# Optimization experiments

Measured on AMD Instinct MI355X. Metric: run time of the kernel, lower is better.

Reference implementation:

```python
import math
import jax, jax.numpy as jnp
import numpy as np
from jax import lax

N, C, H, W = 16, 128, 56, 56


def _conv(x, w, padding, dilation=(1, 1), groups=1):
    # NCHW conv matching torch.nn.Conv2d semantics (bias=False)
    return lax.conv_general_dilated(
        x, w, window_strides=(1, 1),
        padding=[(padding[0], padding[0]), (padding[1], padding[1])],
        rhs_dilation=dilation,
        dimension_numbers=('NCHW', 'OIHW', 'NCHW'),
        feature_group_count=groups)


def setup_inputs() -> dict:
    key = jax.random.key(0)
    ks = jax.random.split(key, 6)
    x = jax.random.normal(ks[0], (N, C, H, W), jnp.float32)
    w2 = jax.random.normal(ks[1], (C, C, 1, 3), jnp.float32) * 0.05   # dense 1x3 conv
    p6w = jax.random.normal(ks[2], (1, C, 7, 1), jnp.float32) * 0.02  # trunc_normal std=0.02
    w7 = jax.random.normal(ks[3], (C, 1, 1, 5), jnp.float32) * 0.05   # depthwise 1x5
    w8 = jax.random.normal(ks[4], (C, 1, 5, 5), jnp.float32) * 0.05   # depthwise 5x5 dil=2
    p9w = jax.random.normal(ks[5], (1, 1, 7, C), jnp.float32) * 0.02
    return {"x": x, "w2": w2, "p6w": p6w, "w7": w7, "w8": w8, "p9w": p9w}


def reference(x, w2, p6w, w7, w8, p9w):
    n, c, h, w = x.shape
    # t_1: F.unfold(x, (1,7), dilation=(1,2), padding=(0,6)) -> (n, c, 7, h, w)
    # tap k reads column j + 2k - 6 of x (zero padded)
    xp = jnp.pad(x, ((0, 0), (0, 0), (0, 0), (6, 6)))
    t1 = jnp.stack([xp[..., 2 * k:2 * k + w] for k in range(7)], axis=2)
    # t_2: dense (1,3) conv, padding (0,1)
    t2 = _conv(x, w2, (0, 1))
    # t_3: windowed channel correlation, (n, c, 7, c)
    t3 = jnp.einsum('nakhw,nbhw->nakb', t1, x) / math.sqrt(h * w)
    # t_4: F.unfold(t_2, (7,1), padding=(3,0)) -> (n, c, 7, h, w), taps along height
    t2p = jnp.pad(t2, ((0, 0), (0, 0), (3, 3), (0, 0)))
    t4 = jnp.stack([t2p[:, :, k:k + h, :] for k in range(7)], axis=2)
    # elementwise weighting
    t6 = p6w * t3          # (1,c,7,1) broadcast over (n,c,7,c)
    # depthwise convs
    t7 = _conv(t2, w7, (0, 2), groups=c)                 # (1,5) depthwise
    t8 = _conv(x, w8, (4, 4), dilation=(2, 2), groups=c)  # (5,5) depthwise, dil 2
    t9 = p9w * t6          # (1,1,7,c) broadcast
    # t_10: contract (c_in, tap) against windowed t4 -> (n, c, h, w)
    t10 = jnp.einsum('nakb,nakhw->nbhw', t9, t4) / math.sqrt(c * 7)
    t11 = t10 - t7
    t12 = t8 - t11
    return t12
```

## Files before the change

kernel.cpp:

```cpp
#include <hip/hip_runtime.h>

#define N_ 16
#define C_ 128
#define H_ 56
#define W_ 56
#define HW_ 3136

typedef __bf16 bf16x8 __attribute__((ext_vector_type(8)));
typedef __bf16 bf16x2 __attribute__((ext_vector_type(2)));
typedef float f32x4 __attribute__((ext_vector_type(4)));

#define XT_PER_N 401408
#define T2_PLANE 3472
#define T2_PER_N 444416
#define S_PER_N 114688
#define T10_PER_N 401408

#define WS_T10_OFF   3670016u
#define WS_T3_OFF    12845056u
#define WS_T2PB_OFF  20185088u
#define WS_W2B_OFF   34406400u

__global__ __launch_bounds__(256) void w2b_prep(const float* __restrict__ w2,
                                                __bf16* __restrict__ w2b) {
    int idx = blockIdx.x * 256 + threadIdx.x;
    int co = idx / 384, kk = idx - co * 384;
    int j = kk >> 7, ci = kk & 127;
    w2b[idx] = (__bf16)w2[co * 384 + ci * 3 + j];
}

__global__ __launch_bounds__(256) void p1_transpose(const float* __restrict__ x,
                                                    __bf16* __restrict__ xT) {
    int c = blockIdx.x, n = blockIdx.y;
    __shared__ float xs[56 * 57];
    int tid = threadIdx.x;
    const float* xp = x + (size_t)(n * C_ + c) * HW_;
    for (int i = tid; i < HW_; i += 256) {
        int h = i / 56, w = i - 56 * h;
        xs[w * 57 + h] = xp[i];
    }
    __syncthreads();
    __bf16* op = xT + (size_t)(n * C_ + c) * HW_;
    for (int i = tid; i < 1568; i += 256) {
        int j = 2 * i;
        int wp = j / 56, h = j - 56 * wp;
        bf16x2 pr = {(__bf16)xs[wp * 57 + h], (__bf16)xs[wp * 57 + h + 1]};
        *(bf16x2*)&op[j] = pr;
    }
}

__global__ __launch_bounds__(256) void k1_mfma(const float* __restrict__ x,
                                               const __bf16* __restrict__ w2b,
                                               __bf16* __restrict__ t2pb) {
    int h = blockIdx.x, n = blockIdx.y;
    __shared__ __align__(16) __bf16 Bs[66 * 136];
    __shared__ __align__(16) __bf16 As[128 * 72];
    int tid = threadIdx.x;
    int wv = tid >> 6, lane = tid & 63;
    int lm = lane & 15, lq = lane >> 4;
    int wi = wv >> 1, wj = wv & 1;

    const float* xn = x + (size_t)n * C_ * HW_ + h * 56;
    for (int i = tid; i < 66 * 128; i += 256) {
        int ci = i / 66, wp = i - 66 * ci;
        int wx = wp - 1;
        float v = (wx >= 0 && wx < 56) ? xn[ci * HW_ + wx] : 0.f;
        Bs[wp * 136 + ci] = (__bf16)v;
    }

    f32x4 acc[4][2];
    f32x4 zero4 = {0.f, 0.f, 0.f, 0.f};
#pragma unroll
    for (int i = 0; i < 4; i++)
#pragma unroll
        for (int j = 0; j < 2; j++) acc[i][j] = zero4;

    const __bf16* w2n = w2b;
    for (int c6 = 0; c6 < 6; c6++) {
#pragma unroll
        for (int u = 0; u < 4; u++) {
            int v = tid + u * 256;
            int m = v & 7, co = v >> 3;
            *(bf16x8*)&As[co * 72 + 8 * m] =
                *(const bf16x8*)(w2n + co * 384 + c6 * 64 + 8 * m);
        }
        __syncthreads();
#pragma unroll
        for (int kl = 0; kl < 2; kl++) {
            int ks = c6 * 2 + kl;
            int j = ks >> 2;
            int cbase = (ks & 3) * 32;
            bf16x8 av[4], bv[2];
#pragma unroll
            for (int i = 0; i < 4; i++)
                av[i] = *(const bf16x8*)&As[(wi * 64 + i * 16 + lm) * 72 + kl * 32 + lq * 8];
#pragma unroll
            for (int jt = 0; jt < 2; jt++) {
                int row = wj * 32 + jt * 16 + lm + j;
                bv[jt] = *(const bf16x8*)&Bs[row * 136 + cbase + lq * 8];
            }
#pragma unroll
            for (int i = 0; i < 4; i++)
#pragma unroll
                for (int jt = 0; jt < 2; jt++)
                    acc[i][jt] = __builtin_amdgcn_mfma_f32_16x16x32_bf16(av[i], bv[jt], acc[i][jt], 0, 0, 0);
        }
        __syncthreads();
    }

    float* buf = (float*)As;
    __bf16* t2n = t2pb + (size_t)n * T2_PER_N;
#pragma unroll 1
    for (int i = 0; i < 4; i++) {
        __syncthreads();
#pragma unroll
        for (int jt = 0; jt < 2; jt++)
#pragma unroll
            for (int r = 0; r < 4; r++)
                buf[(wi * 16 + lq * 4 + r) * 65 + wj * 32 + jt * 16 + lm] = acc[i][jt][r];
        __syncthreads();
        int row = tid >> 3, seg = tid & 7;
        if (seg < 7) {
            int co = (row < 16) ? (i * 16 + row) : (64 + i * 16 + (row - 16));
            const float* src = &buf[row * 65 + seg * 8];
            bf16x8 o8;
#pragma unroll
            for (int d = 0; d < 8; d++) o8[d] = (__bf16)src[d];
            *(bf16x8*)(t2n + (size_t)co * T2_PLANE + (h + 3) * 56 + seg * 8) = o8;
        }
    }
}

__global__ __launch_bounds__(256) void k2_mfma(const __bf16* __restrict__ xT,
                                               float* __restrict__ t3) {
    int hc = blockIdx.x, k = blockIdx.y, n = blockIdx.z;
    __shared__ __align__(16) __bf16 As[128 * 72];
    __shared__ __align__(16) __bf16 Bs[128 * 72];
    int tid = threadIdx.x;
    int wv = tid >> 6, lane = tid & 63;
    int lm = lane & 15, lq = lane >> 4;
    int wi = wv >> 1, wj = wv & 1;

    f32x4 acc[4][4];
    f32x4 zero4 = {0.f, 0.f, 0.f, 0.f};
#pragma unroll
    for (int i = 0; i < 4; i++)
#pragma unroll
        for (int j = 0; j < 4; j++) acc[i][j] = zero4;

    const __bf16* xTn = xT + (size_t)n * XT_PER_N;
    __bf16 bz = (__bf16)0.f;
    bf16x8 vzero = {bz, bz, bz, bz, bz, bz, bz, bz};

    for (int ci = 0; ci < 14; ci++) {
        int w = hc * 14 + ci;
        int wpA = w + 2 * k - 6;
        bool aval = (wpA >= 0 && wpA < 56);
#pragma unroll
        for (int u = 0; u < 4; u++) {
            int v = tid + u * 256;
            int m = v & 7, a = v >> 3;
            bf16x8 va = vzero, vb = vzero;
            if (m < 7) {
                if (aval) va = *(const bf16x8*)(xTn + (a * 56 + wpA) * 56 + 8 * m);
                vb = *(const bf16x8*)(xTn + (a * 56 + w) * 56 + 8 * m);
            }
            *(bf16x8*)&As[a * 72 + 8 * m] = va;
            *(bf16x8*)&Bs[a * 72 + 8 * m] = vb;
        }
        __syncthreads();
#pragma unroll
        for (int kb = 0; kb < 2; kb++) {
            bf16x8 av[4], bv[4];
#pragma unroll
            for (int i = 0; i < 4; i++)
                av[i] = *(const bf16x8*)&As[(wi * 64 + i * 16 + lm) * 72 + kb * 32 + lq * 8];
#pragma unroll
            for (int j = 0; j < 4; j++)
                bv[j] = *(const bf16x8*)&Bs[(wj * 64 + j * 16 + lm) * 72 + kb * 32 + lq * 8];
#pragma unroll
            for (int i = 0; i < 4; i++)
#pragma unroll
                for (int j = 0; j < 4; j++)
                    acc[i][j] = __builtin_amdgcn_mfma_f32_16x16x32_bf16(av[i], bv[j], acc[i][j], 0, 0, 0);
        }
        __syncthreads();
    }

    float* t3p = t3 + (size_t)(n * 7 + k) * (C_ * C_);
    const float inv56 = 1.0f / 56.0f;
#pragma unroll
    for (int i = 0; i < 4; i++)
#pragma unroll
        for (int j = 0; j < 4; j++)
#pragma unroll
            for (int r = 0; r < 4; r++) {
                int a = wi * 64 + i * 16 + lq * 4 + r;
                int b = wj * 64 + j * 16 + lm;
                atomicAdd(&t3p[a * C_ + b], acc[i][j][r] * inv56);
            }
}

__global__ __launch_bounds__(256) void sprep(const float* __restrict__ t3,
                                             const float* __restrict__ p6w,
                                             const float* __restrict__ p9w,
                                             __bf16* __restrict__ s) {
    int idx = blockIdx.x * 256 + threadIdx.x;
    int n = idx / S_PER_N;
    int rem = idx - n * S_PER_N;
    int b = rem / 896;
    int ak = rem - b * 896;
    int a = ak / 7, k = ak - 7 * a;
    const float rs = 0.03340766f;
    float v = t3[((size_t)(n * 7 + k) * C_ + a) * C_ + b] * p6w[a * 7 + k] *
              p9w[k * C_ + b] * rs;
    s[idx] = (__bf16)v;
}

__global__ __launch_bounds__(256) void k3_mfma(const __bf16* __restrict__ s,
                                               const __bf16* __restrict__ t2pb,
                                               __bf16* __restrict__ t10) {
    int tile = blockIdx.x;
    int n = blockIdx.y;
    int hw0 = tile * 64;
    __shared__ __align__(16) __bf16 As[128 * 72];
    __shared__ __align__(16) __bf16 Bs[64 * 72];
    int tid = threadIdx.x;
    int wv = tid >> 6, lane = tid & 63;
    int lm = lane & 15, lq = lane >> 4;
    int wi = wv >> 1, wj = wv & 1;

    f32x4 acc[4][2];
    f32x4 zero4 = {0.f, 0.f, 0.f, 0.f};
#pragma unroll
    for (int i = 0; i < 4; i++)
#pragma unroll
        for (int j = 0; j < 2; j++) acc[i][j] = zero4;

    const __bf16* s_n = s + (size_t)n * S_PER_N;
    const __bf16* t2n = t2pb + (size_t)n * T2_PER_N;

    for (int kb = 0; kb < 14; kb++) {
#pragma unroll
        for (int u = 0; u < 4; u++) {
            int v = tid + u * 256;
            int m = v & 7, b = v >> 3;
            *(bf16x8*)&As[b * 72 + 8 * m] =
                *(const bf16x8*)(s_n + b * 896 + kb * 64 + 8 * m);
        }
        {
            int o = tid & 7;
            int p = tid >> 3;
            int ak0 = kb * 64 + 2 * p;
            int a0 = ak0 / 7, k0 = ak0 - 7 * a0;
            int ak1 = ak0 + 1;
            int a1 = ak1 / 7, k1 = ak1 - 7 * a1;
            int hwg = hw0 + 8 * o;
            bf16x8 v0 = *(const bf16x8*)(t2n + a0 * T2_PLANE + hwg + 56 * k0);
            bf16x8 v1 = *(const bf16x8*)(t2n + a1 * T2_PLANE + hwg + 56 * k1);
            int g = p >> 2;
            int off = (2 * p) & 7;
            int phys = ((g ^ o) << 3) + off;
#pragma unroll
            for (int j = 0; j < 8; j++) {
                int row = 8 * o + j;
                bf16x2 pr = {v0[j], v1[j]};
                *(bf16x2*)&Bs[row * 72 + phys] = pr;
            }
        }
        __syncthreads();
#pragma unroll
        for (int kbi = 0; kbi < 2; kbi++) {
            bf16x8 av[4], bv[2];
#pragma unroll
            for (int i = 0; i < 4; i++)
                av[i] = *(const bf16x8*)&As[(wi * 64 + i * 16 + lm) * 72 + kbi * 32 + lq * 8];
#pragma unroll
            for (int j = 0; j < 2; j++) {
                int row = wj * 32 + j * 16 + lm;
                int g = kbi * 4 + lq;
                int pg = g ^ (row >> 3);
                bv[j] = *(const bf16x8*)&Bs[row * 72 + pg * 8];
            }
#pragma unroll
            for (int i = 0; i < 4; i++)
#pragma unroll
                for (int j = 0; j < 2; j++)
                    acc[i][j] = __builtin_amdgcn_mfma_f32_16x16x32_bf16(av[i], bv[j], acc[i][j], 0, 0, 0);
        }
        __syncthreads();
    }

    float* buf = (float*)As;
    __bf16* t10n = t10 + (size_t)n * T10_PER_N;
#pragma unroll 1
    for (int i = 0; i < 4; i++) {
        __syncthreads();
#pragma unroll
        for (int j = 0; j < 2; j++)
#pragma unroll
            for (int r = 0; r < 4; r++)
                buf[(wi * 16 + lq * 4 + r) * 65 + wj * 32 + j * 16 + lm] = acc[i][j][r];
        __syncthreads();
        int row = tid >> 3, seg = tid & 7;
        int b = (row < 16) ? (i * 16 + row) : (64 + i * 16 + (row - 16));
        const float* src = &buf[row * 65 + seg * 8];
        bf16x8 o8;
#pragma unroll
        for (int d = 0; d < 8; d++) o8[d] = (__bf16)src[d];
        *(bf16x8*)(t10n + (size_t)b * HW_ + hw0 + seg * 8) = o8;
    }
}

__global__ __launch_bounds__(256) void d_final(const float* __restrict__ x,
                                               const __bf16* __restrict__ t2pb,
                                               const __bf16* __restrict__ t10,
                                               const float* __restrict__ w7,
                                               const float* __restrict__ w8,
                                               float* __restrict__ out) {
    int b = blockIdx.x, n = blockIdx.y;
    __shared__ float xs[64 * 65];
    __shared__ float t2s[56 * 60];
    int tid = threadIdx.x;
    const float* xp = x + (size_t)(n * C_ + b) * HW_;
    for (int i = tid; i < 64 * 65; i += 256) {
        int hh = i / 65, ww = i - 65 * hh;
        int h = hh - 4, w = ww - 4;
        float v = (h >= 0 && h < 56 && w >= 0 && w < 56) ? xp[h * 56 + w] : 0.f;
        xs[i] = v;
    }
    const __bf16* t2p = t2pb + (size_t)(n * C_ + b) * T2_PLANE;
    for (int i = tid; i < 56 * 60; i += 256) {
        int h = i / 60, ww = i - 60 * h;
        int w = ww - 2;
        float v = (w >= 0 && w < 56) ? (float)t2p[(h + 3) * 56 + w] : 0.f;
        t2s[i] = v;
    }
    __syncthreads();

    int r = tid >> 2;
    if (r >= 56) return;
    int w0 = (tid & 3) * 14;

    float w7r[5], w8r[25];
#pragma unroll
    for (int q = 0; q < 5; q++) w7r[q] = w7[b * 5 + q];
#pragma unroll
    for (int q = 0; q < 25; q++) w8r[q] = w8[b * 25 + q];

    float acc[14];
    {
        float tw[18];
#pragma unroll
        for (int c = 0; c < 18; c++) tw[c] = t2s[r * 60 + w0 + c];
#pragma unroll
        for (int i = 0; i < 14; i++)
            acc[i] = tw[i] * w7r[0] + tw[i + 1] * w7r[1] + tw[i + 2] * w7r[2] +
                     tw[i + 3] * w7r[3] + tw[i + 4] * w7r[4];
    }
#pragma unroll
    for (int p = 0; p < 5; p++) {
        float xv[22];
        int base = (r + 2 * p) * 65 + w0;
#pragma unroll
        for (int c = 0; c < 22; c++) xv[c] = xs[base + c];
#pragma unroll
        for (int i = 0; i < 14; i++)
            acc[i] += xv[i] * w8r[p * 5 + 0] + xv[i + 2] * w8r[p * 5 + 1] +
                      xv[i + 4] * w8r[p * 5 + 2] + xv[i + 6] * w8r[p * 5 + 3] +
                      xv[i + 8] * w8r[p * 5 + 4];
    }
    const __bf16* t10r = t10 + (size_t)(n * C_ + b) * HW_ + r * 56 + w0;
    float* outr = out + (size_t)(n * C_ + b) * HW_ + r * 56 + w0;
#pragma unroll
    for (int i = 0; i < 14; i++) outr[i] = acc[i] - (float)t10r[i];
}

extern "C" void kernel_launch(void* const* d_in, const int* in_sizes, int n_in,
                              void* d_out, int out_size, void* d_ws, size_t ws_size,
                              hipStream_t stream) {
    const float* x = (const float*)d_in[0];
    const float* w2 = (const float*)d_in[1];
    const float* p6w = (const float*)d_in[2];
    const float* w7 = (const float*)d_in[3];
    const float* w8 = (const float*)d_in[4];
    const float* p9w = (const float*)d_in[5];
    float* outp = (float*)d_out;

    char* ws = (char*)d_ws;
    __bf16* xT = (__bf16*)ws;
    __bf16* s = (__bf16*)ws;
    __bf16* t10 = (__bf16*)(ws + WS_T10_OFF);
    float* t3 = (float*)(ws + WS_T3_OFF);
    __bf16* t2pb = (__bf16*)(ws + WS_T2PB_OFF);
    __bf16* w2b = (__bf16*)(ws + WS_W2B_OFF);

    hipMemsetAsync(t2pb, 0, (size_t)N_ * C_ * T2_PLANE * sizeof(__bf16), stream);
    hipMemsetAsync(t3, 0, (size_t)N_ * 7 * C_ * C_ * sizeof(float), stream);

    w2b_prep<<<dim3(192), 256, 0, stream>>>(w2, w2b);
    p1_transpose<<<dim3(C_, N_), 256, 0, stream>>>(x, xT);
    k1_mfma<<<dim3(H_, N_), 256, 0, stream>>>(x, w2b, t2pb);
    k2_mfma<<<dim3(4, 7, N_), 256, 0, stream>>>(xT, t3);
    sprep<<<dim3((N_ * S_PER_N) / 256), 256, 0, stream>>>(t3, p6w, p9w, s);
    k3_mfma<<<dim3(49, N_), 256, 0, stream>>>(s, t2pb, t10);
    d_final<<<dim3(C_, N_), 256, 0, stream>>>(x, t2pb, t10, w7, w8, outp);
}
```

Baseline: 233.0 us.

## Load MFMA operands directly from global memory and double-buffer k3 B tiles

k1 and k3 now read the A operand (weights or s) straight from global memory into registers instead of staging it through LDS, which removes several barriers. k2 drops LDS staging entirely and walks only the valid, non-padded columns as a flat contiguous range per shift k, doubling the grid to 8 chunks per (k,n). k3 also double-buffers the transposed t2 B tile so the next tile loads while the current one computes. The cost is more uncached-pattern global loads per wave, plus more atomic adds into t3 from the larger k2 grid.

```diff
diff --git a/kernel.cpp b/kernel.cpp
--- a/kernel.cpp
+++ b/kernel.cpp
@@ -54,7 +54,7 @@
                                                __bf16* __restrict__ t2pb) {
     int h = blockIdx.x, n = blockIdx.y;
     __shared__ __align__(16) __bf16 Bs[66 * 136];
-    __shared__ __align__(16) __bf16 As[128 * 72];
+    __shared__ __align__(16) float kbuf[32 * 65];
     int tid = threadIdx.x;
     int wv = tid >> 6, lane = tid & 63;
     int lm = lane & 15, lq = lane >> 4;
@@ -67,6 +67,7 @@
         float v = (wx >= 0 && wx < 56) ? xn[ci * HW_ + wx] : 0.f;
         Bs[wp * 136 + ci] = (__bf16)v;
     }
+    __syncthreads();
 
     f32x4 acc[4][2];
     f32x4 zero4 = {0.f, 0.f, 0.f, 0.f};
@@ -75,40 +76,26 @@
 #pragma unroll
         for (int j = 0; j < 2; j++) acc[i][j] = zero4;
 
-    const __bf16* w2n = w2b;
-    for (int c6 = 0; c6 < 6; c6++) {
-#pragma unroll
-        for (int u = 0; u < 4; u++) {
-            int v = tid + u * 256;
-            int m = v & 7, co = v >> 3;
-            *(bf16x8*)&As[co * 72 + 8 * m] =
-                *(const bf16x8*)(w2n + co * 384 + c6 * 64 + 8 * m);
-        }
-        __syncthreads();
-#pragma unroll
-        for (int kl = 0; kl < 2; kl++) {
-            int ks = c6 * 2 + kl;
-            int j = ks >> 2;
-            int cbase = (ks & 3) * 32;
-            bf16x8 av[4], bv[2];
-#pragma unroll
-            for (int i = 0; i < 4; i++)
-                av[i] = *(const bf16x8*)&As[(wi * 64 + i * 16 + lm) * 72 + kl * 32 + lq * 8];
-#pragma unroll
-            for (int jt = 0; jt < 2; jt++) {
-                int row = wj * 32 + jt * 16 + lm + j;
-                bv[jt] = *(const bf16x8*)&Bs[row * 136 + cbase + lq * 8];
-            }
-#pragma unroll
-            for (int i = 0; i < 4; i++)
-#pragma unroll
-                for (int jt = 0; jt < 2; jt++)
-                    acc[i][jt] = __builtin_amdgcn_mfma_f32_16x16x32_bf16(av[i], bv[jt], acc[i][jt], 0, 0, 0);
-        }
-        __syncthreads();
-    }
-
-    float* buf = (float*)As;
+#pragma unroll 4
+    for (int ks = 0; ks < 12; ks++) {
+        int j = ks >> 2;
+        int cbase = (ks & 3) * 32;
+        bf16x8 av[4], bv[2];
+#pragma unroll
+        for (int i = 0; i < 4; i++)
+            av[i] = *(const bf16x8*)(w2b + (wi * 64 + i * 16 + lm) * 384 + ks * 32 + lq * 8);
+#pragma unroll
+        for (int jt = 0; jt < 2; jt++) {
+            int row = wj * 32 + jt * 16 + lm + j;
+            bv[jt] = *(const bf16x8*)&Bs[row * 136 + cbase + lq * 8];
+        }
+#pragma unroll
+        for (int i = 0; i < 4; i++)
+#pragma unroll
+            for (int jt = 0; jt < 2; jt++)
+                acc[i][jt] = __builtin_amdgcn_mfma_f32_16x16x32_bf16(av[i], bv[jt], acc[i][jt], 0, 0, 0);
+    }
+
     __bf16* t2n = t2pb + (size_t)n * T2_PER_N;
 #pragma unroll 1
     for (int i = 0; i < 4; i++) {
@@ -117,12 +104,12 @@
         for (int jt = 0; jt < 2; jt++)
 #pragma unroll
             for (int r = 0; r < 4; r++)
-                buf[(wi * 16 + lq * 4 + r) * 65 + wj * 32 + jt * 16 + lm] = acc[i][jt][r];
+                kbuf[(wi * 16 + lq * 4 + r) * 65 + wj * 32 + jt * 16 + lm] = acc[i][jt][r];
         __syncthreads();
         int row = tid >> 3, seg = tid & 7;
         if (seg < 7) {
             int co = (row < 16) ? (i * 16 + row) : (64 + i * 16 + (row - 16));
-            const float* src = &buf[row * 65 + seg * 8];
+            const float* src = &kbuf[row * 65 + seg * 8];
             bf16x8 o8;
 #pragma unroll
             for (int d = 0; d < 8; d++) o8[d] = (__bf16)src[d];
@@ -134,8 +121,13 @@
 __global__ __launch_bounds__(256) void k2_mfma(const __bf16* __restrict__ xT,
                                                float* __restrict__ t3) {
     int hc = blockIdx.x, k = blockIdx.y, n = blockIdx.z;
-    __shared__ __align__(16) __bf16 As[128 * 72];
-    __shared__ __align__(16) __bf16 Bs[128 * 72];
+    int w_lo = 6 - 2 * k; if (w_lo < 0) w_lo = 0;
+    int w_hi = 62 - 2 * k; if (w_hi > 56) w_hi = 56;
+    int jlo = w_lo * 56;
+    int L = (w_hi - w_lo) * 56;
+    int T = (L + 63) >> 6;
+    int shiftA = (2 * k - 6) * 56;
+
     int tid = threadIdx.x;
     int wv = tid >> 6, lane = tid & 63;
     int lm = lane & 15, lq = lane >> 4;
@@ -152,39 +144,34 @@
     __bf16 bz = (__bf16)0.f;
     bf16x8 vzero = {bz, bz, bz, bz, bz, bz, bz, bz};
 
-    for (int ci = 0; ci < 14; ci++) {
-        int w = hc * 14 + ci;
-        int wpA = w + 2 * k - 6;
-        bool aval = (wpA >= 0 && wpA < 56);
-#pragma unroll
-        for (int u = 0; u < 4; u++) {
-            int v = tid + u * 256;
-            int m = v & 7, a = v >> 3;
-            bf16x8 va = vzero, vb = vzero;
-            if (m < 7) {
-                if (aval) va = *(const bf16x8*)(xTn + (a * 56 + wpA) * 56 + 8 * m);
-                vb = *(const bf16x8*)(xTn + (a * 56 + w) * 56 + 8 * m);
-            }
-            *(bf16x8*)&As[a * 72 + 8 * m] = va;
-            *(bf16x8*)&Bs[a * 72 + 8 * m] = vb;
-        }
-        __syncthreads();
+    const __bf16* Arow[4];
+    const __bf16* Brow[4];
+#pragma unroll
+    for (int i = 0; i < 4; i++)
+        Arow[i] = xTn + (size_t)(wi * 64 + i * 16 + lm) * HW_ + jlo + shiftA + lq * 8;
+#pragma unroll
+    for (int j = 0; j < 4; j++)
+        Brow[j] = xTn + (size_t)(wj * 64 + j * 16 + lm) * HW_ + jlo + lq * 8;
+
+    for (int c = hc; c < T; c += 8) {
+        int base = c * 64;
 #pragma unroll
         for (int kb = 0; kb < 2; kb++) {
+            int off = base + kb * 32;
+            bool val = (off + lq * 8 + 8 <= L);
             bf16x8 av[4], bv[4];
 #pragma unroll
             for (int i = 0; i < 4; i++)
-                av[i] = *(const bf16x8*)&As[(wi * 64 + i * 16 + lm) * 72 + kb * 32 + lq * 8];
+                av[i] = val ? *(const bf16x8*)(Arow[i] + off) : vzero;
 #pragma unroll
             for (int j = 0; j < 4; j++)
-                bv[j] = *(const bf16x8*)&Bs[(wj * 64 + j * 16 + lm) * 72 + kb * 32 + lq * 8];
+                bv[j] = val ? *(const bf16x8*)(Brow[j] + off) : vzero;
 #pragma unroll
             for (int i = 0; i < 4; i++)
 #pragma unroll
                 for (int j = 0; j < 4; j++)
                     acc[i][j] = __builtin_amdgcn_mfma_f32_16x16x32_bf16(av[i], bv[j], acc[i][j], 0, 0, 0);
         }
-        __syncthreads();
     }
 
     float* t3p = t3 + (size_t)(n * 7 + k) * (C_ * C_);
@@ -223,8 +210,8 @@
     int tile = blockIdx.x;
     int n = blockIdx.y;
     int hw0 = tile * 64;
-    __shared__ __align__(16) __bf16 As[128 * 72];
-    __shared__ __align__(16) __bf16 Bs[64 * 72];
+    __shared__ __align__(16) __bf16 Bs[2][64 * 72];
+    __shared__ __align__(16) float kbuf[32 * 65];
     int tid = threadIdx.x;
     int wv = tid >> 6, lane = tid & 63;
     int lm = lane & 15, lq = lane >> 4;
@@ -240,18 +227,31 @@
     const __bf16* s_n = s + (size_t)n * S_PER_N;
     const __bf16* t2n = t2pb + (size_t)n * T2_PER_N;
 
+    int o = tid & 7;
+    int p = tid >> 3;
+    {
+        int ak0 = 2 * p;
+        int a0 = ak0 / 7, k0 = ak0 - 7 * a0;
+        int ak1 = ak0 + 1;
+        int a1 = ak1 / 7, k1 = ak1 - 7 * a1;
+        int hwg = hw0 + 8 * o;
+        bf16x8 v0 = *(const bf16x8*)(t2n + a0 * T2_PLANE + hwg + 56 * k0);
+        bf16x8 v1 = *(const bf16x8*)(t2n + a1 * T2_PLANE + hwg + 56 * k1);
+        int g = p >> 2;
+        int off = (2 * p) & 7;
+        int phys = ((g ^ o) << 3) + off;
+#pragma unroll
+        for (int j = 0; j < 8; j++) {
+            int row = 8 * o + j;
+            bf16x2 pr = {v0[j], v1[j]};
+            *(bf16x2*)&Bs[0][row * 72 + phys] = pr;
+        }
+    }
+
     for (int kb = 0; kb < 14; kb++) {
-#pragma unroll
-        for (int u = 0; u < 4; u++) {
-            int v = tid + u * 256;
-            int m = v & 7, b = v >> 3;
-            *(bf16x8*)&As[b * 72 + 8 * m] =
-                *(const bf16x8*)(s_n + b * 896 + kb * 64 + 8 * m);
-        }
-        {
-            int o = tid & 7;
-            int p = tid >> 3;
-            int ak0 = kb * 64 + 2 * p;
+        __syncthreads();
+        if (kb + 1 < 14) {
+            int ak0 = (kb + 1) * 64 + 2 * p;
             int a0 = ak0 / 7, k0 = ak0 - 7 * a0;
             int ak1 = ak0 + 1;
             int a1 = ak1 / 7, k1 = ak1 - 7 * a1;
@@ -265,22 +265,22 @@
             for (int j = 0; j < 8; j++) {
                 int row = 8 * o + j;
                 bf16x2 pr = {v0[j], v1[j]};
-                *(bf16x2*)&Bs[row * 72 + phys] = pr;
+                *(bf16x2*)&Bs[(kb + 1) & 1][row * 72 + phys] = pr;
             }
         }
-        __syncthreads();
+        const __bf16* Bcur = Bs[kb & 1];
 #pragma unroll
         for (int kbi = 0; kbi < 2; kbi++) {
             bf16x8 av[4], bv[2];
 #pragma unroll
             for (int i = 0; i < 4; i++)
-                av[i] = *(const bf16x8*)&As[(wi * 64 + i * 16 + lm) * 72 + kbi * 32 + lq * 8];
+                av[i] = *(const bf16x8*)(s_n + (wi * 64 + i * 16 + lm) * 896 + kb * 64 + kbi * 32 + lq * 8);
 #pragma unroll
             for (int j = 0; j < 2; j++) {
                 int row = wj * 32 + j * 16 + lm;
                 int g = kbi * 4 + lq;
                 int pg = g ^ (row >> 3);
-                bv[j] = *(const bf16x8*)&Bs[row * 72 + pg * 8];
+                bv[j] = *(const bf16x8*)&Bcur[row * 72 + pg * 8];
             }
 #pragma unroll
             for (int i = 0; i < 4; i++)
@@ -288,10 +288,8 @@
                 for (int j = 0; j < 2; j++)
                     acc[i][j] = __builtin_amdgcn_mfma_f32_16x16x32_bf16(av[i], bv[j], acc[i][j], 0, 0, 0);
         }
-        __syncthreads();
-    }
-
-    float* buf = (float*)As;
+    }
+
     __bf16* t10n = t10 + (size_t)n * T10_PER_N;
 #pragma unroll 1
     for (int i = 0; i < 4; i++) {
@@ -300,11 +298,11 @@
         for (int j = 0; j < 2; j++)
 #pragma unroll
             for (int r = 0; r < 4; r++)
-                buf[(wi * 16 + lq * 4 + r) * 65 + wj * 32 + j * 16 + lm] = acc[i][j][r];
+                kbuf[(wi * 16 + lq * 4 + r) * 65 + wj * 32 + j * 16 + lm] = acc[i][j][r];
         __syncthreads();
         int row = tid >> 3, seg = tid & 7;
         int b = (row < 16) ? (i * 16 + row) : (64 + i * 16 + (row - 16));
-        const float* src = &buf[row * 65 + seg * 8];
+        const float* src = &kbuf[row * 65 + seg * 8];
         bf16x8 o8;
 #pragma unroll
         for (int d = 0; d < 8; d++) o8[d] = (__bf16)src[d];
@@ -401,7 +399,7 @@
     w2b_prep<<<dim3(192), 256, 0, stream>>>(w2, w2b);
     p1_transpose<<<dim3(C_, N_), 256, 0, stream>>>(x, xT);
     k1_mfma<<<dim3(H_, N_), 256, 0, stream>>>(x, w2b, t2pb);
-    k2_mfma<<<dim3(4, 7, N_), 256, 0, stream>>>(xT, t3);
+    k2_mfma<<<dim3(8, 7, N_), 256, 0, stream>>>(xT, t3);
     sprep<<<dim3((N_ * S_PER_N) / 256), 256, 0, stream>>>(t3, p6w, p9w, s);
     k3_mfma<<<dim3(49, N_), 256, 0, stream>>>(s, t2pb, t10);
     d_final<<<dim3(C_, N_), 256, 0, stream>>>(x, t2pb, t10, w7, w8, outp);
```

After: 299.0 us. 28.3% more time.

## Merge prep and conv/correlation kernels into two combined launches

Applied to the files above, without the earlier changes.

Combines the weight prep and the x transpose into one launch, and folds the zeroing of the t2 padding rows into that launch in place of a full memset. The dense 1x3 conv and the windowed channel correlation now run as two block ranges of a single kernel, so they can execute concurrently. The correlation loop now walks a flattened (w,h) range per tap and skips fully out-of-range columns instead of loading zeros for them. This cuts launch count and memset traffic, at the cost of uneven block workloads inside the fused kernel and extra index logic.

```diff
diff --git a/kernel.cpp b/kernel.cpp
--- a/kernel.cpp
+++ b/kernel.cpp
@@ -21,184 +21,199 @@
 #define WS_T2PB_OFF  20185088u
 #define WS_W2B_OFF   34406400u
 
-__global__ __launch_bounds__(256) void w2b_prep(const float* __restrict__ w2,
-                                                __bf16* __restrict__ w2b) {
-    int idx = blockIdx.x * 256 + threadIdx.x;
-    int co = idx / 384, kk = idx - co * 384;
-    int j = kk >> 7, ci = kk & 127;
-    w2b[idx] = (__bf16)w2[co * 384 + ci * 3 + j];
-}
-
-__global__ __launch_bounds__(256) void p1_transpose(const float* __restrict__ x,
-                                                    __bf16* __restrict__ xT) {
-    int c = blockIdx.x, n = blockIdx.y;
-    __shared__ float xs[56 * 57];
+__global__ __launch_bounds__(256) void f0_prep(const float* __restrict__ x,
+                                               const float* __restrict__ w2,
+                                               __bf16* __restrict__ xT,
+                                               __bf16* __restrict__ w2b,
+                                               __bf16* __restrict__ t2pb) {
+    int bid = blockIdx.x;
     int tid = threadIdx.x;
-    const float* xp = x + (size_t)(n * C_ + c) * HW_;
-    for (int i = tid; i < HW_; i += 256) {
-        int h = i / 56, w = i - 56 * h;
-        xs[w * 57 + h] = xp[i];
-    }
-    __syncthreads();
-    __bf16* op = xT + (size_t)(n * C_ + c) * HW_;
-    for (int i = tid; i < 1568; i += 256) {
-        int j = 2 * i;
-        int wp = j / 56, h = j - 56 * wp;
-        bf16x2 pr = {(__bf16)xs[wp * 57 + h], (__bf16)xs[wp * 57 + h + 1]};
-        *(bf16x2*)&op[j] = pr;
-    }
-}
-
-__global__ __launch_bounds__(256) void k1_mfma(const float* __restrict__ x,
+    if (bid < 2048) {
+        int c = bid & 127, n = bid >> 7;
+        __shared__ float xs[56 * 57];
+        const float* xp = x + (size_t)(n * C_ + c) * HW_;
+        for (int i = tid; i < HW_; i += 256) {
+            int h = i / 56, w = i - 56 * h;
+            xs[w * 57 + h] = xp[i];
+        }
+        __syncthreads();
+        __bf16* op = xT + (size_t)(n * C_ + c) * HW_;
+        for (int i = tid; i < 1568; i += 256) {
+            int j = 2 * i;
+            int wp = j / 56, h = j - 56 * wp;
+            bf16x2 pr = {(__bf16)xs[wp * 57 + h], (__bf16)xs[wp * 57 + h + 1]};
+            *(bf16x2*)&op[j] = pr;
+        }
+        __bf16* tp = t2pb + (size_t)(n * C_ + c) * T2_PLANE;
+        for (int i = tid; i < 336; i += 256)
+            tp[(i < 168) ? i : (3136 + i)] = (__bf16)0.f;
+    } else {
+        int idx = (bid - 2048) * 256 + tid;
+        int co = idx / 384, kk = idx - co * 384;
+        int j = kk >> 7, ci = kk & 127;
+        w2b[idx] = (__bf16)w2[co * 384 + ci * 3 + j];
+    }
+}
+
+__global__ __launch_bounds__(256) void f1_main(const float* __restrict__ x,
                                                const __bf16* __restrict__ w2b,
-                                               __bf16* __restrict__ t2pb) {
-    int h = blockIdx.x, n = blockIdx.y;
-    __shared__ __align__(16) __bf16 Bs[66 * 136];
-    __shared__ __align__(16) __bf16 As[128 * 72];
+                                               const __bf16* __restrict__ xT,
+                                               __bf16* __restrict__ t2pb,
+                                               float* __restrict__ t3) {
+    __shared__ __align__(16) char smem[36864];
+    int bid = blockIdx.x;
     int tid = threadIdx.x;
     int wv = tid >> 6, lane = tid & 63;
     int lm = lane & 15, lq = lane >> 4;
     int wi = wv >> 1, wj = wv & 1;
 
-    const float* xn = x + (size_t)n * C_ * HW_ + h * 56;
-    for (int i = tid; i < 66 * 128; i += 256) {
-        int ci = i / 66, wp = i - 66 * ci;
-        int wx = wp - 1;
-        float v = (wx >= 0 && wx < 56) ? xn[ci * HW_ + wx] : 0.f;
-        Bs[wp * 136 + ci] = (__bf16)v;
-    }
-
-    f32x4 acc[4][2];
-    f32x4 zero4 = {0.f, 0.f, 0.f, 0.f};
-#pragma unroll
-    for (int i = 0; i < 4; i++)
-#pragma unroll
-        for (int j = 0; j < 2; j++) acc[i][j] = zero4;
-
-    const __bf16* w2n = w2b;
-    for (int c6 = 0; c6 < 6; c6++) {
-#pragma unroll
-        for (int u = 0; u < 4; u++) {
-            int v = tid + u * 256;
-            int m = v & 7, co = v >> 3;
-            *(bf16x8*)&As[co * 72 + 8 * m] =
-                *(const bf16x8*)(w2n + co * 384 + c6 * 64 + 8 * m);
-        }
-        __syncthreads();
-#pragma unroll
-        for (int kl = 0; kl < 2; kl++) {
-            int ks = c6 * 2 + kl;
-            int j = ks >> 2;
-            int cbase = (ks & 3) * 32;
-            bf16x8 av[4], bv[2];
-#pragma unroll
-            for (int i = 0; i < 4; i++)
-                av[i] = *(const bf16x8*)&As[(wi * 64 + i * 16 + lm) * 72 + kl * 32 + lq * 8];
-#pragma unroll
-            for (int jt = 0; jt < 2; jt++) {
-                int row = wj * 32 + jt * 16 + lm + j;
-                bv[jt] = *(const bf16x8*)&Bs[row * 136 + cbase + lq * 8];
-            }
-#pragma unroll
-            for (int i = 0; i < 4; i++)
-#pragma unroll
-                for (int jt = 0; jt < 2; jt++)
-                    acc[i][jt] = __builtin_amdgcn_mfma_f32_16x16x32_bf16(av[i], bv[jt], acc[i][jt], 0, 0, 0);
-        }
-        __syncthreads();
-    }
-
-    float* buf = (float*)As;
-    __bf16* t2n = t2pb + (size_t)n * T2_PER_N;
+    if (bid < 448) {
+        int hc = bid & 3;
+        int k = (bid >> 2) % 7;
+        int n = bid / 28;
+        int w_lo = 6 - 2 * k; if (w_lo < 0) w_lo = 0;
+        int w_hi = 62 - 2 * k; if (w_hi > 56) w_hi = 56;
+        int jlo = w_lo * 56;
+        int L = (w_hi - w_lo) * 56;
+        int T = (L + 63) >> 6;
+        int shiftA = (2 * k - 6) * 56;
+
+        __bf16* As = (__bf16*)smem;
+        __bf16* Bs = (__bf16*)(smem + 18432);
+
+        f32x4 acc[4][4];
+        f32x4 zero4 = {0.f, 0.f, 0.f, 0.f};
+#pragma unroll
+        for (int i = 0; i < 4; i++)
+#pragma unroll
+            for (int j = 0; j < 4; j++) acc[i][j] = zero4;
+
+        const __bf16* Ag = xT + (size_t)n * XT_PER_N + jlo + shiftA;
+        const __bf16* Bg = xT + (size_t)n * XT_PER_N + jlo;
+        __bf16 bz = (__bf16)0.f;
+        bf16x8 vzero = {bz, bz, bz, bz, bz, bz, bz, bz};
+
+        for (int c = hc; c < T; c += 4) {
+            int off0 = c * 64;
+#pragma unroll
+            for (int u = 0; u < 4; u++) {
+                int v = tid + u * 256;
+                int m = v & 7, a = v >> 3;
+                int jo = off0 + 8 * m;
+                bool val = (jo + 8 <= L);
+                bf16x8 va = val ? *(const bf16x8*)(Ag + (size_t)a * HW_ + jo) : vzero;
+                bf16x8 vb = val ? *(const bf16x8*)(Bg + (size_t)a * HW_ + jo) : vzero;
+                *(bf16x8*)&As[a * 72 + 8 * m] = va;
+                *(bf16x8*)&Bs[a * 72 + 8 * m] = vb;
+            }
+            __syncthreads();
+#pragma unroll
+            for (int kb = 0; kb < 2; kb++) {
+                bf16x8 av[4], bv[4];
+#pragma unroll
+                for (int i = 0; i < 4; i++)
+                    av[i] = *(const bf16x8*)&As[(wi * 64 + i * 16 + lm) * 72 + kb * 32 + lq * 8];
+#pragma unroll
+                for (int j = 0; j < 4; j++)
+                    bv[j] = *(const bf16x8*)&Bs[(wj * 64 + j * 16 + lm) * 72 + kb * 32 + lq * 8];
+#pragma unroll
+                for (int i = 0; i < 4; i++)
+#pragma unroll
+                    for (int j = 0; j < 4; j++)
+                        acc[i][j] = __builtin_amdgcn_mfma_f32_16x16x32_bf16(av[i], bv[j], acc[i][j], 0, 0, 0);
+            }
+            __syncthreads();
+        }
+
+        float* t3p = t3 + (size_t)(n * 7 + k) * (C_ * C_);
+        const float inv56 = 1.0f / 56.0f;
+#pragma unroll
+        for (int i = 0; i < 4; i++)
+#pragma unroll
+            for (int j = 0; j < 4; j++)
+#pragma unroll
+                for (int r = 0; r < 4; r++) {
+                    int a = wi * 64 + i * 16 + lq * 4 + r;
+                    int b = wj * 64 + j * 16 + lm;
+                    atomicAdd(&t3p[a * C_ + b], acc[i][j][r] * inv56);
+                }
+    } else {
+        int idx = bid - 448;
+        int h = idx % 56, n = idx / 56;
+        __bf16* Bs = (__bf16*)smem;
+        float* kbuf = (float*)(smem + 17952);
+
+        const float* xn = x + (size_t)n * C_ * HW_ + h * 56;
+        for (int i = tid; i < 66 * 128; i += 256) {
+            int ci = i / 66, wp = i - 66 * ci;
+            int wx = wp - 1;
+            float v = (wx >= 0 && wx < 56) ? xn[ci * HW_ + wx] : 0.f;
+            Bs[wp * 136 + ci] = (__bf16)v;
+        }
+
+        f32x4 acc[4][2];
+        f32x4 zero4 = {0.f, 0.f, 0.f, 0.f};
+#pragma unroll
+        for (int i = 0; i < 4; i++)
+#pragma unroll
+            for (int j = 0; j < 2; j++) acc[i][j] = zero4;
+
+        __bf16* Asc = (__bf16*)(smem + 17952);
+        __syncthreads();
+
+        for (int c6 = 0; c6 < 6; c6++) {
+#pragma unroll
+            for (int u = 0; u < 4; u++) {
+                int v = tid + u * 256;
+                int m = v & 7, co = v >> 3;
+                *(bf16x8*)&Asc[co * 72 + 8 * m] =
+                    *(const bf16x8*)(w2b + co * 384 + c6 * 64 + 8 * m);
+            }
+            __syncthreads();
+#pragma unroll
+            for (int kl = 0; kl < 2; kl++) {
+                int ks = c6 * 2 + kl;
+                int j = ks >> 2;
+                int cbase = (ks & 3) * 32;
+                bf16x8 av[4], bv[2];
+#pragma unroll
+                for (int i = 0; i < 4; i++)
+                    av[i] = *(const bf16x8*)&Asc[(wi * 64 + i * 16 + lm) * 72 + kl * 32 + lq * 8];
+#pragma unroll
+                for (int jt = 0; jt < 2; jt++) {
+                    int row = wj * 32 + jt * 16 + lm + j;
+                    bv[jt] = *(const bf16x8*)&Bs[row * 136 + cbase + lq * 8];
+                }
+#pragma unroll
+                for (int i = 0; i < 4; i++)
+#pragma unroll
+                    for (int jt = 0; jt < 2; jt++)
+                        acc[i][jt] = __builtin_amdgcn_mfma_f32_16x16x32_bf16(av[i], bv[jt], acc[i][jt], 0, 0, 0);
+            }
+            __syncthreads();
+        }
+
+        __bf16* t2n = t2pb + (size_t)n * T2_PER_N;
 #pragma unroll 1
-    for (int i = 0; i < 4; i++) {
-        __syncthreads();
-#pragma unroll
-        for (int jt = 0; jt < 2; jt++)
-#pragma unroll
-            for (int r = 0; r < 4; r++)
-                buf[(wi * 16 + lq * 4 + r) * 65 + wj * 32 + jt * 16 + lm] = acc[i][jt][r];
-        __syncthreads();
-        int row = tid >> 3, seg = tid & 7;
-        if (seg < 7) {
-            int co = (row < 16) ? (i * 16 + row) : (64 + i * 16 + (row - 16));
-            const float* src = &buf[row * 65 + seg * 8];
-            bf16x8 o8;
-#pragma unroll
-            for (int d = 0; d < 8; d++) o8[d] = (__bf16)src[d];
-            *(bf16x8*)(t2n + (size_t)co * T2_PLANE + (h + 3) * 56 + seg * 8) = o8;
-        }
-    }
-}
-
-__global__ __launch_bounds__(256) void k2_mfma(const __bf16* __restrict__ xT,
-                                               float* __restrict__ t3) {
-    int hc = blockIdx.x, k = blockIdx.y, n = blockIdx.z;
-    __shared__ __align__(16) __bf16 As[128 * 72];
-    __shared__ __align__(16) __bf16 Bs[128 * 72];
-    int tid = threadIdx.x;
-    int wv = tid >> 6, lane = tid & 63;
-    int lm = lane & 15, lq = lane >> 4;
-    int wi = wv >> 1, wj = wv & 1;
-
-    f32x4 acc[4][4];
-    f32x4 zero4 = {0.f, 0.f, 0.f, 0.f};
-#pragma unroll
-    for (int i = 0; i < 4; i++)
-#pragma unroll
-        for (int j = 0; j < 4; j++) acc[i][j] = zero4;
-
-    const __bf16* xTn = xT + (size_t)n * XT_PER_N;
-    __bf16 bz = (__bf16)0.f;
-    bf16x8 vzero = {bz, bz, bz, bz, bz, bz, bz, bz};
-
-    for (int ci = 0; ci < 14; ci++) {
-        int w = hc * 14 + ci;
-        int wpA = w + 2 * k - 6;
-        bool aval = (wpA >= 0 && wpA < 56);
-#pragma unroll
-        for (int u = 0; u < 4; u++) {
-            int v = tid + u * 256;
-            int m = v & 7, a = v >> 3;
-            bf16x8 va = vzero, vb = vzero;
-            if (m < 7) {
-                if (aval) va = *(const bf16x8*)(xTn + (a * 56 + wpA) * 56 + 8 * m);
-                vb = *(const bf16x8*)(xTn + (a * 56 + w) * 56 + 8 * m);
-            }
-            *(bf16x8*)&As[a * 72 + 8 * m] = va;
-            *(bf16x8*)&Bs[a * 72 + 8 * m] = vb;
-        }
-        __syncthreads();
-#pragma unroll
-        for (int kb = 0; kb < 2; kb++) {
-            bf16x8 av[4], bv[4];
-#pragma unroll
-            for (int i = 0; i < 4; i++)
-                av[i] = *(const bf16x8*)&As[(wi * 64 + i * 16 + lm) * 72 + kb * 32 + lq * 8];
-#pragma unroll
-            for (int j = 0; j < 4; j++)
-                bv[j] = *(const bf16x8*)&Bs[(wj * 64 + j * 16 + lm) * 72 + kb * 32 + lq * 8];
-#pragma unroll
-            for (int i = 0; i < 4; i++)
-#pragma unroll
-                for (int j = 0; j < 4; j++)
-                    acc[i][j] = __builtin_amdgcn_mfma_f32_16x16x32_bf16(av[i], bv[j], acc[i][j], 0, 0, 0);
-        }
-        __syncthreads();
-    }
-
-    float* t3p = t3 + (size_t)(n * 7 + k) * (C_ * C_);
-    const float inv56 = 1.0f / 56.0f;
-#pragma unroll
-    for (int i = 0; i < 4; i++)
-#pragma unroll
-        for (int j = 0; j < 4; j++)
-#pragma unroll
-            for (int r = 0; r < 4; r++) {
-                int a = wi * 64 + i * 16 + lq * 4 + r;
-                int b = wj * 64 + j * 16 + lm;
-                atomicAdd(&t3p[a * C_ + b], acc[i][j][r] * inv56);
-            }
+        for (int i = 0; i < 4; i++) {
+            __syncthreads();
+#pragma unroll
+            for (int jt = 0; jt < 2; jt++)
+#pragma unroll
+                for (int r = 0; r < 4; r++)
+                    kbuf[(wi * 16 + lq * 4 + r) * 65 + wj * 32 + jt * 16 + lm] = acc[i][jt][r];
+            __syncthreads();
+            int row = tid >> 3, seg = tid & 7;
+            if (seg < 7) {
+                int co = (row < 16) ? (i * 16 + row) : (64 + i * 16 + (row - 16));
+                const float* src = &kbuf[row * 65 + seg * 8];
+                bf16x8 o8;
+#pragma unroll
+                for (int d = 0; d < 8; d++) o8[d] = (__bf16)src[d];
+                *(bf16x8*)(t2n + (size_t)co * T2_PLANE + (h + 3) * 56 + seg * 8) = o8;
+            }
+        }
+    }
 }
 
 __global__ __launch_bounds__(256) void sprep(const float* __restrict__ t3,
@@ -395,13 +410,10 @@
     __bf16* t2pb = (__bf16*)(ws + WS_T2PB_OFF);
     __bf16* w2b = (__bf16*)(ws + WS_W2B_OFF);
 
-    hipMemsetAsync(t2pb, 0, (size_t)N_ * C_ * T2_PLANE * sizeof(__bf16), stream);
     hipMemsetAsync(t3, 0, (size_t)N_ * 7 * C_ * C_ * sizeof(float), stream);
 
-    w2b_prep<<<dim3(192), 256, 0, stream>>>(w2, w2b);
-    p1_transpose<<<dim3(C_, N_), 256, 0, stream>>>(x, xT);
-    k1_mfma<<<dim3(H_, N_), 256, 0, stream>>>(x, w2b, t2pb);
-    k2_mfma<<<dim3(4, 7, N_), 256, 0, stream>>>(xT, t3);
+    f0_prep<<<dim3(2240), 256, 0, stream>>>(x, w2, xT, w2b, t2pb);
+    f1_main<<<dim3(1344), 256, 0, stream>>>(x, w2b, xT, t2pb, t3);
     sprep<<<dim3((N_ * S_PER_N) / 256), 256, 0, stream>>>(t3, p6w, p9w, s);
     k3_mfma<<<dim3(49, N_), 256, 0, stream>>>(s, t2pb, t10);
     d_final<<<dim3(C_, N_), 256, 0, stream>>>(x, t2pb, t10, w7, w8, outp);
```

Measured after the change: 221.2 us. 5.1% less time.
